# Kernel tuning notes

Hardware: AMD Instinct MI355X
Metric: run time of the kernel (lower is better)

The kernel has to match this reference:

```python
import jax, jax.numpy as jnp
import numpy as np

DELTA = 1.0 / 1024.0  # init kwarg `delta`


def _lin_init(key, out_f, in_f):
    k1, k2 = jax.random.split(key)
    s = 1.0 / np.sqrt(in_f)
    w = jax.random.uniform(k1, (out_f, in_f), minval=-s, maxval=s, dtype=jnp.float32)
    b = jax.random.uniform(k2, (out_f,), minval=-s, maxval=s, dtype=jnp.float32)
    return w, b


def setup_inputs() -> dict:
    key = jax.random.key(0)
    B, S, C, H, T = 262144, 64, 8, 64, 1024  # batch, state_dim, control_dim, rnn hidden, seq len
    ks = jax.random.split(key, 12)
    t = jax.random.uniform(ks[0], (B, 1), dtype=jnp.float32)            # in [0,1) -> t_u in [0,T)
    x = jax.random.normal(ks[1], (B, S), dtype=jnp.float32)
    u = jax.random.normal(ks[2], (T, C), dtype=jnp.float32)
    i2h_w, i2h_b = _lin_init(ks[3], H, C + H)
    h2o_w, h2o_b = _lin_init(ks[4], S, C + H)
    xw1, xb1 = _lin_init(ks[5], 20, 1 + S)
    xw2, xb2 = _lin_init(ks[6], 20, 20)
    xw3, xb3 = _lin_init(ks[7], S, 20)
    uw1, ub1 = _lin_init(ks[8], 20, 1 + S)
    uw2, ub2 = _lin_init(ks[9], 20, 20)
    uw3, ub3 = _lin_init(ks[10], S, 20)
    cw, cb = _lin_init(ks[11], S, 2 * S)
    return {"t": t, "x": x, "u": u,
            "i2h_w": i2h_w, "i2h_b": i2h_b, "h2o_w": h2o_w, "h2o_b": h2o_b,
            "xw1": xw1, "xb1": xb1, "xw2": xw2, "xb2": xb2, "xw3": xw3, "xb3": xb3,
            "uw1": uw1, "ub1": ub1, "uw2": uw2, "ub2": ub2, "uw3": uw3, "ub3": ub3,
            "cw": cw, "cb": cb}


def _mlp(z, w1, b1, w2, b2, w3, b3):
    h = jax.nn.sigmoid(z @ w1.T + b1)
    h = jax.nn.sigmoid(h @ w2.T + b2)
    return h @ w3.T + b3


def reference(t, x, u, i2h_w, i2h_b, h2o_w, h2o_b,
              xw1, xb1, xw2, xb2, xw3, xb3,
              uw1, ub1, uw2, ub2, uw3, ub3, cw, cb):
    # state branch: x_dnn([t, x])
    state_part = _mlp(jnp.concatenate([t, x], axis=1), xw1, xb1, xw2, xb2, xw3, xb3)

    # sequential tanh-RNN over the control sequence (hidden starts at zero)
    hsz = i2h_w.shape[0]

    def step(h, u_k):
        j = jnp.concatenate([u_k, h])                 # (C+H,)
        h_new = jnp.tanh(j @ i2h_w.T + i2h_b)         # (H,)
        out = jnp.tanh(j @ h2o_w.T + h2o_b)           # (S,)
        return h_new, out

    h0 = jnp.zeros((hsz,), dtype=u.dtype)
    _, u_rnn_out = jax.lax.scan(step, h0, u)          # (T, S)

    # gather encoded controls per query time
    t_u = jnp.floor(t / DELTA).astype(jnp.int32).squeeze(-1)  # (B,)
    encoded_controls = u_rnn_out[t_u]                 # (B, S)

    control_part = _mlp(jnp.concatenate([t, encoded_controls], axis=1),
                        uw1, ub1, uw2, ub2, uw3, ub3)

    stacked = jax.nn.sigmoid(jnp.concatenate([state_part, control_part], axis=1))  # (B, 2S)
    return stacked @ cw.T + cb
```

## Files before the change

### kernel.cpp

```cpp
#include <hip/hip_runtime.h>
#include <hip/hip_bf16.h>

#define T_SEQ 1024
#define CHUNK 64
#define NCHUNK 16

__device__ __forceinline__ float fast_sigmoid(float x) {
    return 1.0f / (1.0f + __expf(-x));
}
__device__ __forceinline__ float fast_tanh(float x) {
    float e = __expf(2.0f * x);
    return 1.0f - 2.0f / (e + 1.0f);
}

__device__ __forceinline__ float quad_sum(float x) {
    int y1 = __builtin_amdgcn_mov_dpp(__float_as_int(x), 0xB1, 0xF, 0xF, true);
    float s1 = x + __int_as_float(y1);
    int y2 = __builtin_amdgcn_mov_dpp(__float_as_int(s1), 0x4E, 0xF, 0xF, true);
    return s1 + __int_as_float(y2);
}

__global__ __launch_bounds__(256) void k_rnn_pre(
    const float* __restrict__ u,
    const float* __restrict__ i2h_w, const float* __restrict__ i2h_b,
    const float* __restrict__ h2o_w, const float* __restrict__ h2o_b,
    float* __restrict__ pre_i, float* __restrict__ pre_o) {
    int idx = blockIdx.x * 256 + threadIdx.x;
    int k = idx >> 6, i = idx & 63;
    float a = i2h_b[i], b = h2o_b[i];
#pragma unroll
    for (int c = 0; c < 8; ++c) {
        float uv = u[k * 8 + c];
        a += uv * i2h_w[i * 72 + c];
        b += uv * h2o_w[i * 72 + c];
    }
    pre_i[idx] = a;
    pre_o[idx] = b;
}

__global__ __launch_bounds__(64) void k_rnn_out(
    const float* __restrict__ h2o_w,
    const float* __restrict__ pre_o,
    const float* __restrict__ hseq,
    float* __restrict__ uout) {
    int k = blockIdx.x, i = threadIdx.x;
    __shared__ float hk[64];
    hk[i] = hseq[k * 64 + i];
    __syncthreads();
    float acc = pre_o[k * 64 + i];
#pragma unroll
    for (int m = 0; m < 64; ++m) acc += h2o_w[i * 72 + 8 + m] * hk[m];
    uout[k * 64 + i] = fast_tanh(acc);
}

#define L_XW1 0
#define L_UW1 1360
#define L_XW2 2720
#define L_UW2 3120
#define L_XW3 3520
#define L_UW3 4800
#define L_CWT 6080
#define L_XB1 14272
#define L_XB2 14292
#define L_UB1 14312
#define L_UB2 14332
#define L_XB3 14352
#define L_UB3 14416
#define L_CB  14480
#define L_TOT 14544

__global__ __launch_bounds__(256) void k_repack(
    const float* __restrict__ xw1, const float* __restrict__ uw1,
    const float* __restrict__ xw2, const float* __restrict__ uw2,
    const float* __restrict__ xw3, const float* __restrict__ uw3,
    const float* __restrict__ cw,
    const float* __restrict__ xb1, const float* __restrict__ xb2,
    const float* __restrict__ ub1, const float* __restrict__ ub2,
    const float* __restrict__ xb3, const float* __restrict__ ub3,
    const float* __restrict__ cb, float* __restrict__ wp) {
    int i = blockIdx.x * 256 + threadIdx.x;
    if (i >= L_TOT) return;
    float v = 0.0f;
    if (i < 1360) {
        int o = i / 68, c = i - o * 68;
        if (c == 0) v = xw1[o * 65];
        else if (c >= 4) v = xw1[o * 65 + c - 3];
    } else if (i < 2720) {
        int j = i - 1360; int o = j / 68, c = j - o * 68;
        if (c == 0) v = uw1[o * 65];
        else if (c >= 4) v = uw1[o * 65 + c - 3];
    } else if (i < 3120) v = xw2[i - 2720];
    else if (i < 3520) v = uw2[i - 3120];
    else if (i < 4800) v = xw3[i - 3520];
    else if (i < 6080) v = uw3[i - 4800];
    else if (i < 14272) {
        int j = i - 6080; int row = j >> 6, s = j & 63;
        v = cw[s * 128 + row];
    }
    else if (i < 14292) v = xb1[i - 14272];
    else if (i < 14312) v = xb2[i - 14292];
    else if (i < 14332) v = ub1[i - 14312];
    else if (i < 14352) v = ub2[i - 14332];
    else if (i < 14416) v = xb3[i - 14352];
    else if (i < 14480) v = ub3[i - 14416];
    else v = cb[i - 14480];
    wp[i] = v;
}

template <int OW1, int OB1, int OW2, int OB2>
__device__ __forceinline__ void mlp20(const float* __restrict__ sm,
                                      float tval, const float4* z, float* h2) {
    float h1[20];
#pragma unroll 4
    for (int o = 0; o < 20; ++o) {
        const int ro = OW1 + o * 68;
        float a = sm[OB1 + o] + tval * sm[ro];
        const float4* wr = reinterpret_cast<const float4*>(&sm[ro + 4]);
#pragma unroll
        for (int v = 0; v < 16; ++v) {
            float4 w4 = wr[v];
            a += z[v].x * w4.x + z[v].y * w4.y + z[v].z * w4.z + z[v].w * w4.w;
        }
        h1[o] = fast_sigmoid(a);
    }
#pragma unroll 4
    for (int o = 0; o < 20; ++o) {
        float a = sm[OB2 + o];
        const float4* wr = reinterpret_cast<const float4*>(&sm[OW2 + o * 20]);
#pragma unroll
        for (int v = 0; v < 5; ++v) {
            float4 w4 = wr[v];
            a += h1[4*v+0]*w4.x + h1[4*v+1]*w4.y + h1[4*v+2]*w4.z + h1[4*v+3]*w4.w;
        }
        h2[o] = fast_sigmoid(a);
    }
}

template <int OW3, int OB3, int OCWT>
__device__ __forceinline__ void final64(const float* __restrict__ sm,
                                        const float* h2, float* oacc) {
#pragma unroll 2
    for (int o = 0; o < 64; ++o) {
        float a = sm[OB3 + o];
        const float4* wr = reinterpret_cast<const float4*>(&sm[OW3 + o * 20]);
#pragma unroll
        for (int v = 0; v < 5; ++v) {
            float4 w4 = wr[v];
            a += h2[4*v+0]*w4.x + h2[4*v+1]*w4.y + h2[4*v+2]*w4.z + h2[4*v+3]*w4.w;
        }
        float s = fast_sigmoid(a);
        const float4* cr = reinterpret_cast<const float4*>(&sm[OCWT + o * 64]);
#pragma unroll
        for (int v = 0; v < 16; ++v) {
            float4 c4 = cr[v];
            oacc[4*v+0] += s * c4.x; oacc[4*v+1] += s * c4.y;
            oacc[4*v+2] += s * c4.z; oacc[4*v+3] += s * c4.w;
        }
    }
}

#define SMEMF_MAIN 14544

__global__ __launch_bounds__(256) void k_main(
    const float* __restrict__ t_in, const float* __restrict__ x_in,
    const float* __restrict__ i2h_w,
    const float* __restrict__ pre_i,
    const float* __restrict__ wp,
    float* __restrict__ hseq, float* __restrict__ out) {
    __shared__ float smem[SMEMF_MAIN];
    const int tid = threadIdx.x;
    const int bid = blockIdx.x;

    if (bid == 0) {
        float* pre2 = smem;
        float* hs   = smem + 8192;
        const int lane = tid & 63;
        const int wv = tid >> 6;
        const int t = lane >> 2;
        const int j = lane & 3;
        const int o = 16 * wv + t;

        float wih[16];
#pragma unroll
        for (int jj = 0; jj < 16; ++jj) wih[jj] = i2h_w[o * 72 + 8 + 16 * j + jj];

        {
            const float4* pg = reinterpret_cast<const float4*>(pre_i);
            float4* pd = reinterpret_cast<float4*>(pre2);
#pragma unroll
            for (int q = 0; q < 4; ++q) pd[tid * 4 + q] = pg[tid * 4 + q];
        }
        if (tid < 64) hs[tid] = 0.0f;
        __syncthreads();
        float4 pl0, pl1, pl2, pl3;

        for (int c = 0; c < NCHUNK; ++c) {
            const float* pre_c = pre2 + (c & 1) * 4096;
            if (c + 1 < NCHUNK) {
                const float4* pg = reinterpret_cast<const float4*>(pre_i + (c + 1) * 4096);
                pl0 = pg[tid*4+0]; pl1 = pg[tid*4+1]; pl2 = pg[tid*4+2]; pl3 = pg[tid*4+3];
            }
            for (int s = 0; s < CHUNK; ++s) {
                const float4* hb = reinterpret_cast<const float4*>(hs + s * 64) + 4 * j;
                float4 b0 = hb[0], b1 = hb[1], b2 = hb[2], b3 = hb[3];
                float pre_v = pre_c[s * 64 + o];
                float a0 = wih[ 0]*b0.x + wih[ 1]*b0.y + wih[ 2]*b0.z + wih[ 3]*b0.w;
                float a1 = wih[ 4]*b1.x + wih[ 5]*b1.y + wih[ 6]*b1.z + wih[ 7]*b1.w;
                float a2 = wih[ 8]*b2.x + wih[ 9]*b2.y + wih[10]*b2.z + wih[11]*b2.w;
                float a3 = wih[12]*b3.x + wih[13]*b3.y + wih[14]*b3.z + wih[15]*b3.w;
                float tot = quad_sum((a0 + a1) + (a2 + a3));
                float hn = fast_tanh(tot + pre_v);
                if (j == 0) hs[(s + 1) * 64 + o] = hn;
                __syncthreads();
            }
            {
                const float4* hsrc = reinterpret_cast<const float4*>(hs);
                float4* hdst = reinterpret_cast<float4*>(hseq + c * 4096);
#pragma unroll
                for (int q = 0; q < 4; ++q) hdst[tid * 4 + q] = hsrc[tid * 4 + q];
            }
            if (c + 1 < NCHUNK) {
                float4* pd = reinterpret_cast<float4*>(pre2 + ((c + 1) & 1) * 4096);
                pd[tid*4+0] = pl0; pd[tid*4+1] = pl1; pd[tid*4+2] = pl2; pd[tid*4+3] = pl3;
            }
            __syncthreads();
            if (tid < 64) hs[tid] = hs[4096 + tid];
            __syncthreads();
        }
        return;
    }

    {
        float4* s4 = reinterpret_cast<float4*>(smem);
        const float4* w4 = reinterpret_cast<const float4*>(wp);
        for (int idx = tid; idx < L_TOT / 4; idx += 256) s4[idx] = w4[idx];
    }
    __syncthreads();

    const int r = (bid - 1) * 256 + tid;
    float tval = t_in[r];
    float4 z[16];
    const float4* xp = reinterpret_cast<const float4*>(x_in + (size_t)r * 64);
#pragma unroll
    for (int v = 0; v < 16; ++v) z[v] = xp[v];

    float h2[20];
    mlp20<L_XW1, L_XB1, L_XW2, L_XB2>(smem, tval, z, h2);

    float oacc[64];
    {
        const float4* cbp = reinterpret_cast<const float4*>(&smem[L_CB]);
#pragma unroll
        for (int v = 0; v < 16; ++v) {
            float4 c4 = cbp[v];
            oacc[4*v+0] = c4.x; oacc[4*v+1] = c4.y;
            oacc[4*v+2] = c4.z; oacc[4*v+3] = c4.w;
        }
    }
    final64<L_XW3, L_XB3, L_CWT>(smem, h2, oacc);

    float4* op = reinterpret_cast<float4*>(out + (size_t)r * 64);
#pragma unroll
    for (int v = 0; v < 16; ++v) {
        float4 f;
        f.x = oacc[4*v+0]; f.y = oacc[4*v+1];
        f.z = oacc[4*v+2]; f.w = oacc[4*v+3];
        op[v] = f;
    }
}

__global__ __launch_bounds__(256) void k_ctrl(
    const float* __restrict__ t_in, const float* __restrict__ uo,
    const float* __restrict__ wp, float* __restrict__ out) {
    __shared__ float sm[L_TOT];
    const int tid = threadIdx.x;
    {
        float4* s4 = reinterpret_cast<float4*>(sm);
        const float4* w4 = reinterpret_cast<const float4*>(wp);
        for (int idx = tid; idx < L_TOT / 4; idx += 256) s4[idx] = w4[idx];
    }
    __syncthreads();

    const int r = blockIdx.x * 256 + tid;
    float tval = t_in[r];
    int ti = min((int)(tval * 1024.0f), 1023);
    float4 z[16];
    const float4* ep = reinterpret_cast<const float4*>(uo + ti * 64);
#pragma unroll
    for (int v = 0; v < 16; ++v) z[v] = ep[v];

    float h2[20];
    mlp20<L_UW1, L_UB1, L_UW2, L_UB2>(sm, tval, z, h2);

    float oacc[64];
    float4* op = reinterpret_cast<float4*>(out + (size_t)r * 64);
#pragma unroll
    for (int v = 0; v < 16; ++v) {
        float4 f = op[v];
        oacc[4*v+0] = f.x; oacc[4*v+1] = f.y;
        oacc[4*v+2] = f.z; oacc[4*v+3] = f.w;
    }
    final64<L_UW3, L_UB3, L_CWT + 64 * 64>(sm, h2, oacc);
#pragma unroll
    for (int v = 0; v < 16; ++v) {
        float4 f;
        f.x = oacc[4*v+0]; f.y = oacc[4*v+1];
        f.z = oacc[4*v+2]; f.w = oacc[4*v+3];
        op[v] = f;
    }
}

extern "C" void kernel_launch(void* const* d_in, const int* in_sizes, int n_in,
                              void* d_out, int out_size, void* d_ws, size_t ws_size,
                              hipStream_t stream) {
    const float* t     = (const float*)d_in[0];
    const float* x     = (const float*)d_in[1];
    const float* u     = (const float*)d_in[2];
    const float* i2h_w = (const float*)d_in[3];
    const float* i2h_b = (const float*)d_in[4];
    const float* h2o_w = (const float*)d_in[5];
    const float* h2o_b = (const float*)d_in[6];
    const float* xw1 = (const float*)d_in[7];  const float* xb1 = (const float*)d_in[8];
    const float* xw2 = (const float*)d_in[9];  const float* xb2 = (const float*)d_in[10];
    const float* xw3 = (const float*)d_in[11]; const float* xb3 = (const float*)d_in[12];
    const float* uw1 = (const float*)d_in[13]; const float* ub1 = (const float*)d_in[14];
    const float* uw2 = (const float*)d_in[15]; const float* ub2 = (const float*)d_in[16];
    const float* uw3 = (const float*)d_in[17]; const float* ub3 = (const float*)d_in[18];
    const float* cw  = (const float*)d_in[19]; const float* cb  = (const float*)d_in[20];
    float* out = (float*)d_out;

    float* ws = (float*)d_ws;
    float* pre_i = ws;
    float* uo    = ws;
    float* pre_o = ws + 65536;
    float* hseq  = ws + 131072;
    float* wp    = ws + 196608;

    int Bv = in_sizes[0];

    hipLaunchKernelGGL(k_repack, dim3((L_TOT + 255) / 256), dim3(256), 0, stream,
                       xw1, uw1, xw2, uw2, xw3, uw3, cw,
                       xb1, xb2, ub1, ub2, xb3, ub3, cb, wp);
    hipLaunchKernelGGL(k_rnn_pre, dim3(256), dim3(256), 0, stream,
                       u, i2h_w, i2h_b, h2o_w, h2o_b, pre_i, pre_o);
    hipLaunchKernelGGL(k_main, dim3(1 + Bv / 256), dim3(256), 0, stream,
                       t, x, i2h_w, pre_i, wp, hseq, out);
    hipLaunchKernelGGL(k_rnn_out, dim3(T_SEQ), dim3(64), 0, stream,
                       h2o_w, pre_o, hseq, uo);
    hipLaunchKernelGGL(k_ctrl, dim3(Bv / 256), dim3(256), 0, stream,
                       t, uo, wp, out);
}
```

Before: 355.1 us.

## Defer state-branch output layer to ctrl kernel, staging 20-wide hidden in output buffer

```diff
diff --git a/kernel.cpp b/kernel.cpp
--- a/kernel.cpp
+++ b/kernel.cpp
@@ -38,36 +38,44 @@
     pre_o[idx] = b;
 }
 
-__global__ __launch_bounds__(64) void k_rnn_out(
+__global__ __launch_bounds__(256) void k_rnn_out(
     const float* __restrict__ h2o_w,
     const float* __restrict__ pre_o,
     const float* __restrict__ hseq,
     float* __restrict__ uout) {
-    int k = blockIdx.x, i = threadIdx.x;
-    __shared__ float hk[64];
-    hk[i] = hseq[k * 64 + i];
+    const int tid = threadIdx.x;
+    const int sub = tid >> 6, i = tid & 63;
+    const int k = blockIdx.x * 4 + sub;
+    __shared__ float hk[4][64];
+    hk[sub][i] = hseq[k * 64 + i];
     __syncthreads();
     float acc = pre_o[k * 64 + i];
-#pragma unroll
-    for (int m = 0; m < 64; ++m) acc += h2o_w[i * 72 + 8 + m] * hk[m];
+    const float4* h4 = reinterpret_cast<const float4*>(hk[sub]);
+#pragma unroll
+    for (int v = 0; v < 16; ++v) {
+        float4 hv = h4[v];
+        acc += h2o_w[i * 72 + 8 + 4*v+0] * hv.x + h2o_w[i * 72 + 8 + 4*v+1] * hv.y
+             + h2o_w[i * 72 + 8 + 4*v+2] * hv.z + h2o_w[i * 72 + 8 + 4*v+3] * hv.w;
+    }
     uout[k * 64 + i] = fast_tanh(acc);
 }
 
-#define L_XW1 0
-#define L_UW1 1360
-#define L_XW2 2720
-#define L_UW2 3120
-#define L_XW3 3520
-#define L_UW3 4800
-#define L_CWT 6080
-#define L_XB1 14272
-#define L_XB2 14292
-#define L_UB1 14312
-#define L_UB2 14332
-#define L_XB3 14352
-#define L_UB3 14416
-#define L_CB  14480
-#define L_TOT 14544
+#define P_SW1 0
+#define P_SB1 1360
+#define P_SW2 1380
+#define P_SB2 1780
+#define P_SML 1800
+#define P_UW1 1800
+#define P_UB1 3160
+#define P_UW2 3180
+#define P_UB2 3580
+#define P_XW3 3600
+#define P_XB3 4880
+#define P_UW3 4944
+#define P_UB3 6224
+#define P_CWT 6288
+#define P_CB  14480
+#define P_TOT 14544
 
 __global__ __launch_bounds__(256) void k_repack(
     const float* __restrict__ xw1, const float* __restrict__ uw1,
@@ -79,30 +87,30 @@
     const float* __restrict__ xb3, const float* __restrict__ ub3,
     const float* __restrict__ cb, float* __restrict__ wp) {
     int i = blockIdx.x * 256 + threadIdx.x;
-    if (i >= L_TOT) return;
+    if (i >= P_TOT) return;
     float v = 0.0f;
     if (i < 1360) {
         int o = i / 68, c = i - o * 68;
         if (c == 0) v = xw1[o * 65];
         else if (c >= 4) v = xw1[o * 65 + c - 3];
-    } else if (i < 2720) {
-        int j = i - 1360; int o = j / 68, c = j - o * 68;
+    } else if (i < 1380) v = xb1[i - 1360];
+    else if (i < 1780) v = xw2[i - 1380];
+    else if (i < 1800) v = xb2[i - 1780];
+    else if (i < 3160) {
+        int j = i - 1800; int o = j / 68, c = j - o * 68;
         if (c == 0) v = uw1[o * 65];
         else if (c >= 4) v = uw1[o * 65 + c - 3];
-    } else if (i < 3120) v = xw2[i - 2720];
-    else if (i < 3520) v = uw2[i - 3120];
-    else if (i < 4800) v = xw3[i - 3520];
-    else if (i < 6080) v = uw3[i - 4800];
-    else if (i < 14272) {
-        int j = i - 6080; int row = j >> 6, s = j & 63;
+    } else if (i < 3180) v = ub1[i - 3160];
+    else if (i < 3580) v = uw2[i - 3180];
+    else if (i < 3600) v = ub2[i - 3580];
+    else if (i < 4880) v = xw3[i - 3600];
+    else if (i < 4944) v = xb3[i - 4880];
+    else if (i < 6224) v = uw3[i - 4944];
+    else if (i < 6288) v = ub3[i - 6224];
+    else if (i < 14480) {
+        int j = i - 6288; int row = j >> 6, s = j & 63;
         v = cw[s * 128 + row];
     }
-    else if (i < 14292) v = xb1[i - 14272];
-    else if (i < 14312) v = xb2[i - 14292];
-    else if (i < 14332) v = ub1[i - 14312];
-    else if (i < 14352) v = ub2[i - 14332];
-    else if (i < 14416) v = xb3[i - 14352];
-    else if (i < 14480) v = ub3[i - 14416];
     else v = cb[i - 14480];
     wp[i] = v;
 }
@@ -233,7 +241,7 @@
     {
         float4* s4 = reinterpret_cast<float4*>(smem);
         const float4* w4 = reinterpret_cast<const float4*>(wp);
-        for (int idx = tid; idx < L_TOT / 4; idx += 256) s4[idx] = w4[idx];
+        for (int idx = tid; idx < P_SML / 4; idx += 256) s4[idx] = w4[idx];
     }
     __syncthreads();
 
@@ -245,11 +253,52 @@
     for (int v = 0; v < 16; ++v) z[v] = xp[v];
 
     float h2[20];
-    mlp20<L_XW1, L_XB1, L_XW2, L_XB2>(smem, tval, z, h2);
+    mlp20<P_SW1, P_SB1, P_SW2, P_SB2>(smem, tval, z, h2);
+
+    float4* op = reinterpret_cast<float4*>(out + (size_t)r * 64);
+#pragma unroll
+    for (int v = 0; v < 5; ++v) {
+        float4 f;
+        f.x = h2[4*v+0]; f.y = h2[4*v+1]; f.z = h2[4*v+2]; f.w = h2[4*v+3];
+        op[v] = f;
+    }
+}
+
+__global__ __launch_bounds__(256) void k_ctrl(
+    const float* __restrict__ t_in, const float* __restrict__ uo,
+    const float* __restrict__ wp, float* __restrict__ out) {
+    __shared__ float sm[P_TOT];
+    const int tid = threadIdx.x;
+    {
+        float4* s4 = reinterpret_cast<float4*>(sm);
+        const float4* w4 = reinterpret_cast<const float4*>(wp);
+        for (int idx = tid; idx < P_TOT / 4; idx += 256) s4[idx] = w4[idx];
+    }
+    __syncthreads();
+
+    const int r = blockIdx.x * 256 + tid;
+    float4* op = reinterpret_cast<float4*>(out + (size_t)r * 64);
+
+    float h2s[20];
+#pragma unroll
+    for (int v = 0; v < 5; ++v) {
+        float4 f = op[v];
+        h2s[4*v+0] = f.x; h2s[4*v+1] = f.y; h2s[4*v+2] = f.z; h2s[4*v+3] = f.w;
+    }
+
+    float tval = t_in[r];
+    int ti = min((int)(tval * 1024.0f), 1023);
+    float4 z[16];
+    const float4* ep = reinterpret_cast<const float4*>(uo + ti * 64);
+#pragma unroll
+    for (int v = 0; v < 16; ++v) z[v] = ep[v];
+
+    float h2c[20];
+    mlp20<P_UW1, P_UB1, P_UW2, P_UB2>(sm, tval, z, h2c);
 
     float oacc[64];
     {
-        const float4* cbp = reinterpret_cast<const float4*>(&smem[L_CB]);
+        const float4* cbp = reinterpret_cast<const float4*>(&sm[P_CB]);
 #pragma unroll
         for (int v = 0; v < 16; ++v) {
             float4 c4 = cbp[v];
@@ -257,50 +306,9 @@
             oacc[4*v+2] = c4.z; oacc[4*v+3] = c4.w;
         }
     }
-    final64<L_XW3, L_XB3, L_CWT>(smem, h2, oacc);
-
-    float4* op = reinterpret_cast<float4*>(out + (size_t)r * 64);
-#pragma unroll
-    for (int v = 0; v < 16; ++v) {
-        float4 f;
-        f.x = oacc[4*v+0]; f.y = oacc[4*v+1];
-        f.z = oacc[4*v+2]; f.w = oacc[4*v+3];
-        op[v] = f;
-    }
-}
-
-__global__ __launch_bounds__(256) void k_ctrl(
-    const float* __restrict__ t_in, const float* __restrict__ uo,
-    const float* __restrict__ wp, float* __restrict__ out) {
-    __shared__ float sm[L_TOT];
-    const int tid = threadIdx.x;
-    {
-        float4* s4 = reinterpret_cast<float4*>(sm);
-        const float4* w4 = reinterpret_cast<const float4*>(wp);
-        for (int idx = tid; idx < L_TOT / 4; idx += 256) s4[idx] = w4[idx];
-    }
-    __syncthreads();
-
-    const int r = blockIdx.x * 256 + tid;
-    float tval = t_in[r];
-    int ti = min((int)(tval * 1024.0f), 1023);
-    float4 z[16];
-    const float4* ep = reinterpret_cast<const float4*>(uo + ti * 64);
-#pragma unroll
-    for (int v = 0; v < 16; ++v) z[v] = ep[v];
-
-    float h2[20];
-    mlp20<L_UW1, L_UB1, L_UW2, L_UB2>(sm, tval, z, h2);
-
-    float oacc[64];
-    float4* op = reinterpret_cast<float4*>(out + (size_t)r * 64);
-#pragma unroll
-    for (int v = 0; v < 16; ++v) {
-        float4 f = op[v];
-        oacc[4*v+0] = f.x; oacc[4*v+1] = f.y;
-        oacc[4*v+2] = f.z; oacc[4*v+3] = f.w;
-    }
-    final64<L_UW3, L_UB3, L_CWT + 64 * 64>(sm, h2, oacc);
+    final64<P_XW3, P_XB3, P_CWT>(sm, h2s, oacc);
+    final64<P_UW3, P_UB3, P_CWT + 64 * 64>(sm, h2c, oacc);
+
 #pragma unroll
     for (int v = 0; v < 16; ++v) {
         float4 f;
@@ -338,14 +346,14 @@
 
     int Bv = in_sizes[0];
 
-    hipLaunchKernelGGL(k_repack, dim3((L_TOT + 255) / 256), dim3(256), 0, stream,
+    hipLaunchKernelGGL(k_repack, dim3((P_TOT + 255) / 256), dim3(256), 0, stream,
                        xw1, uw1, xw2, uw2, xw3, uw3, cw,
                        xb1, xb2, ub1, ub2, xb3, ub3, cb, wp);
     hipLaunchKernelGGL(k_rnn_pre, dim3(256), dim3(256), 0, stream,
                        u, i2h_w, i2h_b, h2o_w, h2o_b, pre_i, pre_o);
     hipLaunchKernelGGL(k_main, dim3(1 + Bv / 256), dim3(256), 0, stream,
                        t, x, i2h_w, pre_i, wp, hseq, out);
-    hipLaunchKernelGGL(k_rnn_out, dim3(T_SEQ), dim3(64), 0, stream,
+    hipLaunchKernelGGL(k_rnn_out, dim3(T_SEQ / 4), dim3(256), 0, stream,
                        h2o_w, pre_o, hseq, uo);
     hipLaunchKernelGGL(k_ctrl, dim3(Bv / 256), dim3(256), 0, stream,
                        t, uo, wp, out);
```

After: 428.7 us. 1.21x slower.
